# Kernel optimization log

Measured on AMD Instinct MI355X. Metric: run time of the kernel, lower is better.

The kernel has to match this reference:

```python
import jax, jax.numpy as jnp
import numpy as np

# ---- module constants (from init_kwargs / zounds.SR22050) ----
SEQ = 64
N_SAMPLES = 16384
N_EVENTS = 16
N_HARM = 32
NOISE_WS = 512
NOISE_STEP = 256
NYQ = 11025.0  # SR22050 nyquist
MIN_F0 = 20.0 / NYQ
MAX_F0 = 800.0 / NYQ
F0_DIFF = MAX_F0 - MIN_F0
HARM_FACTOR = jnp.arange(2, 2 + N_HARM, dtype=jnp.float32)  # [2..33]


def lin_interp(x, size):
    """torch F.interpolate(mode='linear', align_corners=False) along last dim."""
    L = x.shape[-1]
    pos = (jnp.arange(size, dtype=x.dtype) + 0.5) * (L / size) - 0.5
    pos = jnp.clip(pos, 0.0, L - 1)
    i0 = jnp.floor(pos).astype(jnp.int32)
    i1 = jnp.minimum(i0 + 1, L - 1)
    w = (pos - i0).astype(x.dtype)
    return x[..., i0] * (1.0 - w) + x[..., i1] * w


def band_filtered_noise(noise_frames, mean, std):
    """Per-frame Gaussian band-pass of white noise in the STFT domain, overlap-add.
    noise_frames: (b,e,F,ws); mean/std: (b,e,F) in normalized freq [0,1]."""
    ws = noise_frames.shape[-1]
    n = jnp.arange(ws, dtype=noise_frames.dtype)
    win = 0.5 - 0.5 * jnp.cos(2.0 * jnp.pi * n / ws)  # Hann
    spec = jnp.fft.rfft(noise_frames * win, axis=-1)  # (b,e,F,ws//2+1)
    freqs = jnp.linspace(0.0, 1.0, ws // 2 + 1)
    filt = jnp.exp(-0.5 * ((freqs[None, None, None, :] - mean[..., None]) / std[..., None]) ** 2)
    frames = jnp.fft.irfft(spec * filt, n=ws, axis=-1)  # (b,e,F,ws)
    # overlap-add with hop NOISE_STEP (ws == 2*step -> two half-chunks per frame)
    b, e, Fn, _ = frames.shape
    chunks = frames.reshape(b, e, Fn, 2, NOISE_STEP)
    a = chunks[..., 0, :].reshape(b, e, Fn * NOISE_STEP)
    c = chunks[..., 1, :].reshape(b, e, Fn * NOISE_STEP)
    out = jnp.zeros((b, e, (Fn + 1) * NOISE_STEP), dtype=frames.dtype)
    out = out.at[..., : Fn * NOISE_STEP].add(a)
    out = out.at[..., NOISE_STEP:].add(c)
    return out[..., :N_SAMPLES]


def setup_inputs() -> dict:
    key = jax.random.key(0)
    ks = jax.random.split(key, 8)
    B = 8
    return {
        "f0": jax.random.uniform(ks[0], (B, N_EVENTS, SEQ), jnp.float32),
        "overall_env": jax.random.uniform(ks[1], (B, N_EVENTS, SEQ), jnp.float32),
        "osc_env": jax.random.uniform(ks[2], (B, N_EVENTS, SEQ), jnp.float32),
        "noise_env": jax.random.uniform(ks[3], (B, N_EVENTS, SEQ), jnp.float32),
        "harm_env": jax.random.uniform(ks[4], (B, N_EVENTS, N_HARM, SEQ), jnp.float32),
        "noise_std": jax.random.uniform(ks[5], (B, N_EVENTS, SEQ), jnp.float32),
        "f0_baselines": jax.random.uniform(ks[6], (B, N_EVENTS, 1), jnp.float32),
        "noise_frames": jax.random.normal(ks[7], (B, N_EVENTS, SEQ, NOISE_WS), jnp.float32),
    }


def reference(f0, overall_env, osc_env, noise_env, harm_env, noise_std, f0_baselines, noise_frames):
    # f0_baselines branch (ERB-scaled deviation around baseline)
    f0 = jnp.clip(f0, -0.5, 0.5)
    scaled_erb = (0.108 * (f0_baselines * NYQ) + 24.7) / NYQ
    f0 = f0_baselines + f0 * scaled_erb

    orig_f0 = f0 = jnp.clip(f0, 0.0, 1.0)
    overall_env = jnp.clip(overall_env, 0.0, 1.0)
    osc_env = jnp.clip(osc_env, 0.0, 1.0)
    harm_env = jnp.clip(harm_env, 0.0, 1.0)
    noise_std = jnp.clip(noise_std, 1e-12, 1.0)

    f0n = MIN_F0 + f0 * F0_DIFF                                   # (b,e,S)
    harm_f = f0n[:, :, None, :] * HARM_FACTOR[None, None, :, None]  # (b,e,H,S)
    harm_env = osc_env[:, :, None, :] * harm_env                  # (b,e,H,S)

    fund = lin_interp(f0n, N_SAMPLES)           # (b,e,N)
    harm_f_i = lin_interp(harm_f, N_SAMPLES)    # (b,e,H,N)
    osc_env_i = lin_interp(osc_env, N_SAMPLES)  # (b,e,N)
    harm_env_i = lin_interp(harm_env, N_SAMPLES)

    fundamental = jnp.sin(jnp.cumsum(fund * jnp.pi, axis=-1)) * osc_env_i
    harmonics = (jnp.sin(jnp.cumsum(harm_f_i * jnp.pi, axis=-1)) * harm_env_i).sum(axis=-2)
    osc = fundamental + harmonics

    noise_mean = MIN_F0 + orig_f0 * F0_DIFF
    nstd = noise_std * F0_DIFF
    noise = band_filtered_noise(noise_frames, noise_mean, nstd)

    osc_mix = lin_interp(overall_env, N_SAMPLES)
    noise_mix = lin_interp(1.0 - overall_env, N_SAMPLES)
    return osc * osc_mix + noise * noise_mix
```

## Files before the change

kernel.cpp:

```cpp
#include <hip/hip_runtime.h>
#include <math.h>

#define SEQ 64
#define NSAMP 16384
#define NHARM 32
#define NWS 512
#define NSTEP 256
#define BE 128
#define NFRAMES 8192

typedef _Float16 half8 __attribute__((ext_vector_type(8)));
typedef float f32x4 __attribute__((ext_vector_type(4)));

__device__ __forceinline__ float sin_rev(float x) {
  float r; asm("v_sin_f32 %0, %1" : "=v"(r) : "v"(x)); return r;
}
__device__ __forceinline__ float cos_rev(float x) {
  float r; asm("v_cos_f32 %0, %1" : "=v"(r) : "v"(x)); return r;
}
__device__ __forceinline__ float clip01(float v) { return fminf(fmaxf(v, 0.0f), 1.0f); }

__device__ __forceinline__ float f0_to_norm(float f0v, float bl) {
  const float NYQ = 11025.0f;
  const float MIN_F0 = 20.0f / 11025.0f;
  const float F0_DIFF = 780.0f / 11025.0f;
  float v = fminf(fmaxf(f0v, -0.5f), 0.5f);
  float erb = (0.108f * (bl * NYQ) + 24.7f) / NYQ;
  float fv = clip01(bl + v * erb);
  return MIN_F0 + fv * F0_DIFF;
}

__global__ __launch_bounds__(256) void prep_k(_Float16* __restrict__ W1) {
  const int m = blockIdx.x, k = m & 127;
  const int tid = threadIdx.x;
  const bool isSin = m >= 128;
  for (int n = tid; n < 512; n += 256) {
    int a = (k * n) & 511;
    float ph = (float)a * (1.0f / 512.0f);
    W1[m * 512 + n] = (_Float16)(isSin ? sin_rev(ph) : cos_rev(ph));
  }
}

__global__ __launch_bounds__(256) void gemmf_k(const float* __restrict__ Af,
                                               const _Float16* __restrict__ B,
                                               _Float16* __restrict__ Cout,
                                               _Float16* __restrict__ W2,
                                               const float* __restrict__ f0,
                                               const float* __restrict__ nstd,
                                               const float* __restrict__ f0b) {
  const int tid = threadIdx.x;

  if (blockIdx.x < 256) {
    const int k = tid & 127;
    const bool isSin = tid >= 128;
#pragma unroll
    for (int rr = 0; rr < 2; ++rr) {
      const int n = blockIdx.x * 2 + rr;
      int a = (k * n) & 511;
      float ph = (float)a * (1.0f / 512.0f);
      W2[n * 256 + tid] = (_Float16)(isSin ? sin_rev(ph) : cos_rev(ph));
    }
    return;
  }

  const int p = blockIdx.x - 256;
  const int x = p & 7, j = p >> 3;
  const int mstripe = ((j >> 2) << 3) + x;
  const int bn0 = (j & 3) * 64;
  const int m0 = mstripe * 32;

  const int Kt = 512;
  const int wave = tid >> 6, lane = tid & 63;
  const int r = lane & 15, q = lane >> 4;
  const int wr = (wave & 1) * 16;
  const int wc = (wave >> 1) * 32;
  __shared__ __align__(16) _Float16 Ash[2][32 * 64];
  __shared__ __align__(16) _Float16 Bsh[2][64 * 64];
  __shared__ __align__(16) float whann[512];

  const int nT = Kt >> 6;
  const int srowA = tid >> 3;
  const int srowB0 = tid >> 3, srowB1 = (256 + tid) >> 3;
  const int skg = tid & 7;

  half8 ra, rb[2];
  f32x4 acc[2] = {};

  whann[tid] = 0.5f - 0.5f * cos_rev((float)tid * (1.0f / 512.0f));
  whann[tid + 256] = 0.5f - 0.5f * cos_rev((float)(tid + 256) * (1.0f / 512.0f));
  __syncthreads();

  auto load_a = [&](int kk) {
    const float* s0 = Af + (size_t)(m0 + srowA) * Kt + kk + skg * 8;
    float4 a0 = ((const float4*)s0)[0], a1 = ((const float4*)s0)[1];
    float4 w0 = *(const float4*)(&whann[kk + skg * 8]);
    float4 w1 = *(const float4*)(&whann[kk + skg * 8 + 4]);
    ra[0] = (_Float16)(a0.x * w0.x); ra[1] = (_Float16)(a0.y * w0.y);
    ra[2] = (_Float16)(a0.z * w0.z); ra[3] = (_Float16)(a0.w * w0.w);
    ra[4] = (_Float16)(a1.x * w1.x); ra[5] = (_Float16)(a1.y * w1.y);
    ra[6] = (_Float16)(a1.z * w1.z); ra[7] = (_Float16)(a1.w * w1.w);
    rb[0] = *(const half8*)(B + (size_t)(bn0 + srowB0) * Kt + kk + skg * 8);
    rb[1] = *(const half8*)(B + (size_t)(bn0 + srowB1) * Kt + kk + skg * 8);
  };
  auto store_lds = [&](int b) {
    *(half8*)(&Ash[b][srowA * 64 + ((skg ^ (srowA & 7)) << 3)]) = ra;
    *(half8*)(&Bsh[b][srowB0 * 64 + ((skg ^ (srowB0 & 7)) << 3)]) = rb[0];
    *(half8*)(&Bsh[b][srowB1 * 64 + ((skg ^ (srowB1 & 7)) << 3)]) = rb[1];
  };

  load_a(0);
  store_lds(0);

  for (int t = 0;;) {
    if (t + 1 < nT) load_a((t + 1) << 6);
    __syncthreads();
    const int b = t & 1;
#pragma unroll
    for (int ks = 0; ks < 2; ++ks) {
      const int kg = ks * 4 + q;
      const int ar = wr + r;
      half8 af = *(const half8*)(&Ash[b][ar * 64 + ((kg ^ (ar & 7)) << 3)]);
#pragma unroll
      for (int ni = 0; ni < 2; ++ni) {
        const int br = wc + ni * 16 + r;
        half8 bf = *(const half8*)(&Bsh[b][br * 64 + ((kg ^ (br & 7)) << 3)]);
        acc[ni] = __builtin_amdgcn_mfma_f32_16x16x32_f16(af, bf, acc[ni], 0, 0, 0);
      }
    }
    if (t + 1 >= nT) break;
    __syncthreads();
    store_lds((t + 1) & 1);
    ++t;
  }

  const float F0_DIFF = 780.0f / 11025.0f;
#pragma unroll
  for (int reg = 0; reg < 4; ++reg) {
    const int row = m0 + wr + q * 4 + reg;
    const float mu = f0_to_norm(f0[row], f0b[row >> 6]);
    const float sd = fminf(fmaxf(nstd[row], 1e-12f), 1.0f) * F0_DIFF;
    const float inv_sd = 1.0f / sd;
    const float a = inv_sd * (1.0f / 256.0f);
    const float bmu = mu * inv_sd;
#pragma unroll
    for (int ni = 0; ni < 2; ++ni) {
      const int col = bn0 + wc + ni * 16 + r;
      const int k = col & 127;
      float z = fmaf((float)k, a, -bmu);
      float cf = (k == 0) ? (1.0f / 512.0f) : (2.0f / 512.0f);
      float s = cf * exp2f(z * z * -0.72134752044f);
      Cout[(size_t)row * 256 + col] = (_Float16)(acc[ni][reg] * s);
    }
  }
}

__global__ __launch_bounds__(256) void invfin_k(const _Float16* __restrict__ AB,
                                                const _Float16* __restrict__ W2,
                                                const float* __restrict__ f0,
                                                const float* __restrict__ f0b,
                                                const float* __restrict__ oenv_g,
                                                const float* __restrict__ oscenv_g,
                                                const float* __restrict__ henv_g,
                                                float* __restrict__ out) {
  const int p = blockIdx.x;
  const int x = p & 7, j = p >> 3;
  const int be = ((j >> 3) << 3) + x;
  const int sub = j & 7;
  const int chalf = sub >> 2;
  const int n0 = (sub & 3) * 64;
  const int m0c = be * 64 + chalf * 32;
  const int tid = threadIdx.x;
  const int wave = tid >> 6, lane = tid & 63;
  const int r = lane & 15, q = lane >> 4;
  const int wr = (wave & 1) * 16;
  const int wc = (wave >> 1) * 32;

  __shared__ __align__(16) _Float16 A2sh[33 * 64];
  __shared__ __align__(16) _Float16 B1sh[64 * 64];
  __shared__ __align__(16) _Float16 B2sh[64 * 64];
  __shared__ __align__(16) float4 qe4[8 * SEQ];
  __shared__ float oenv[SEQ], oscE[SEQ];
  __shared__ float Fs[SEQ], Ds[SEQ], Gs[SEQ];

  if (tid < SEQ) {
    oenv[tid] = clip01(oenv_g[be * SEQ + tid]);
    oscE[tid] = clip01(oscenv_g[be * SEQ + tid]);
    Fs[tid] = f0_to_norm(f0[be * SEQ + tid], f0b[be]);
  }
  __syncthreads();

  if (tid < SEQ) {
    const int s = tid;
    float fcur = Fs[s];
    float fnxt = (s < 63) ? Fs[s + 1] : Fs[63];
    Ds[s] = fnxt - fcur;
    double term = 128.0 * ((double)fcur + (double)fnxt);
    double sc = term;
#pragma unroll
    for (int off = 1; off < 64; off <<= 1) {
      double u = __shfl_up(sc, off, 64);
      if (s >= off) sc += u;
    }
    double C = 128.0 * (double)Fs[0] + (sc - term);
    Gs[s] = (float)(C - 2.0 * floor(C * 0.5));
  }

  for (int idx = tid; idx < 8 * SEQ; idx += 256) {
    int hq = idx >> 6, s = idx & 63;
    const float* hb = henv_g + (size_t)be * (NHARM * SEQ) + (4 * hq) * SEQ + s;
    float e = oscE[s];
    qe4[idx] = make_float4(e * clip01(hb[0]), e * clip01(hb[64]),
                           e * clip01(hb[128]), e * clip01(hb[192]));
  }

  auto stage_AB = [&](int kk) {
#pragma unroll
    for (int it = 0; it < 2; ++it) {
      int g = it * 256 + tid;
      if (g < 264) {
        int row = g >> 3, kg = g & 7;
        half8 v = {0, 0, 0, 0, 0, 0, 0, 0};
        if (row > 0 || chalf == 1)
          v = *(const half8*)(AB + (size_t)(m0c - 1 + row) * 256 + kk + kg * 8);
        *(half8*)(&A2sh[row * 64 + ((kg ^ (row & 7)) << 3)]) = v;
      }
    }
#pragma unroll
    for (int it = 0; it < 4; ++it) {
      int g = it * 256 + tid;
      int row = (g >> 3) & 63, kg = g & 7;
      bool second = g >= 512;
      int wrow = n0 + row + (second ? 256 : 0);
      half8 v = *(const half8*)(W2 + (size_t)wrow * 256 + kk + kg * 8);
      _Float16* dst = second ? B2sh : B1sh;
      *(half8*)(&dst[row * 64 + ((kg ^ (row & 7)) << 3)]) = v;
    }
  };

  f32x4 acc[2] = {};
  stage_AB(0);
  __syncthreads();

  for (int t = 0;;) {
#pragma unroll
    for (int ks = 0; ks < 2; ++ks) {
      const int kg = ks * 4 + q;
      const int ra1 = 1 + wr + r;
      const int ra2 = wr + r;
      half8 af1 = *(const half8*)(&A2sh[ra1 * 64 + ((kg ^ (ra1 & 7)) << 3)]);
      half8 af2 = *(const half8*)(&A2sh[ra2 * 64 + ((kg ^ (ra2 & 7)) << 3)]);
#pragma unroll
      for (int ni = 0; ni < 2; ++ni) {
        const int rb = wc + ni * 16 + r;
        const int sw = (kg ^ (rb & 7)) << 3;
        half8 bf1 = *(const half8*)(&B1sh[rb * 64 + sw]);
        half8 bf2 = *(const half8*)(&B2sh[rb * 64 + sw]);
        acc[ni] = __builtin_amdgcn_mfma_f32_16x16x32_f16(af1, bf1, acc[ni], 0, 0, 0);
        acc[ni] = __builtin_amdgcn_mfma_f32_16x16x32_f16(af2, bf2, acc[ni], 0, 0, 0);
      }
    }
    if (t == 3) break;
    __syncthreads();
    stage_AB((t + 1) << 6);
    __syncthreads();
    ++t;
  }

#pragma unroll
  for (int reg = 0; reg < 4; ++reg) {
    const int c = chalf * 32 + wr + q * 4 + reg;
#pragma unroll
    for (int ni = 0; ni < 2; ++ni) {
      const int n = n0 + wc + ni * 16 + r;
      const int t = c * 256 + n;
      float pos = ((float)t + 0.5f) * (1.0f / 256.0f) - 0.5f;
      pos = fminf(fmaxf(pos, 0.0f), 63.0f);
      int i0 = (int)pos;
      int i1 = min(i0 + 1, 63);
      float w = pos - (float)i0;

      float pph;
      if (t < 128) {
        pph = (float)(t + 1) * Fs[0];
      } else {
        int s = (t - 128) >> 8;
        float u1 = (float)((t - 128) - (s << 8) + 1);
        pph = Gs[s] + fmaf(Ds[s] * (1.0f / 512.0f), u1 * u1, u1 * Fs[s]);
      }
      pph = pph - 2.0f * floorf(pph * 0.5f);
      float xv = pph * 0.5f;
      float sb = sin_rev(xv);
      float cb = cos_rev(xv);
      float C = 2.0f * cb;

      float fund = sb * (oscE[i0] * (1.0f - w) + oscE[i1] * w);
      float d0 = 0.0f, d1 = 0.0f;
      float sp = sb;
      float scur = C * sb;
#pragma unroll
      for (int hq = 0; hq < 8; ++hq) {
        float4 qa = qe4[hq * 64 + i0];
        float4 qb = qe4[hq * 64 + i1];
        d0 = fmaf(scur, qa.x, d0); d1 = fmaf(scur, qb.x, d1);
        sp = fmaf(C, scur, -sp);
        d0 = fmaf(sp, qa.y, d0);   d1 = fmaf(sp, qb.y, d1);
        scur = fmaf(C, sp, -scur);
        d0 = fmaf(scur, qa.z, d0); d1 = fmaf(scur, qb.z, d1);
        sp = fmaf(C, scur, -sp);
        d0 = fmaf(sp, qa.w, d0);   d1 = fmaf(sp, qb.w, d1);
        scur = fmaf(C, sp, -scur);
      }
      float osc = fund + d0 * (1.0f - w) + d1 * w;
      float mix = oenv[i0] * (1.0f - w) + oenv[i1] * w;
      out[(size_t)be * NSAMP + t] = fmaf(osc, mix, acc[ni][reg] * (1.0f - mix));
    }
  }
}

extern "C" void kernel_launch(void* const* d_in, const int* in_sizes, int n_in,
                              void* d_out, int out_size, void* d_ws, size_t ws_size,
                              hipStream_t stream) {
  const float* f0           = (const float*)d_in[0];
  const float* overall_env  = (const float*)d_in[1];
  const float* osc_env      = (const float*)d_in[2];
  const float* harm_env     = (const float*)d_in[4];
  const float* noise_std    = (const float*)d_in[5];
  const float* f0_base      = (const float*)d_in[6];
  const float* noise_frames = (const float*)d_in[7];
  float* out = (float*)d_out;

  _Float16* W1 = (_Float16*)d_ws;
  _Float16* W2 = W1 + 256 * 512;
  _Float16* AB = W2 + 512 * 256;

  prep_k<<<256, 256, 0, stream>>>(W1);
  gemmf_k<<<1280, 256, 0, stream>>>(noise_frames, W1, AB, W2, f0, noise_std, f0_base);
  invfin_k<<<1024, 256, 0, stream>>>(
      AB, W2, f0, f0_base, overall_env, osc_env, harm_env, out);
}
```

Baseline: 34.54 us.

## Generate DFT twiddles inline in forward GEMM and prefetch inverse GEMM tiles

Removes the separate prep kernel that wrote the forward DFT matrix to global memory. The forward GEMM now computes its cos/sin B-tile values on the fly with hardware sin/cos instructions while the A tile is being loaded. Separately, the inverse GEMM staging is split into a global-load phase issued before the MFMA loop and an LDS-write phase afterward, so loads overlap compute. This saves a kernel launch and global traffic but adds 16 transcendental ops per thread per tile in the forward GEMM.

```diff
diff --git a/kernel.cpp b/kernel.cpp
--- a/kernel.cpp
+++ b/kernel.cpp
@@ -30,19 +30,7 @@
   return MIN_F0 + fv * F0_DIFF;
 }
 
-__global__ __launch_bounds__(256) void prep_k(_Float16* __restrict__ W1) {
-  const int m = blockIdx.x, k = m & 127;
-  const int tid = threadIdx.x;
-  const bool isSin = m >= 128;
-  for (int n = tid; n < 512; n += 256) {
-    int a = (k * n) & 511;
-    float ph = (float)a * (1.0f / 512.0f);
-    W1[m * 512 + n] = (_Float16)(isSin ? sin_rev(ph) : cos_rev(ph));
-  }
-}
-
 __global__ __launch_bounds__(256) void gemmf_k(const float* __restrict__ Af,
-                                               const _Float16* __restrict__ B,
                                                _Float16* __restrict__ Cout,
                                                _Float16* __restrict__ W2,
                                                const float* __restrict__ f0,
@@ -89,6 +77,11 @@
   whann[tid] = 0.5f - 0.5f * cos_rev((float)tid * (1.0f / 512.0f));
   whann[tid + 256] = 0.5f - 0.5f * cos_rev((float)(tid + 256) * (1.0f / 512.0f));
   __syncthreads();
+
+  const int kB0 = (bn0 + srowB0) & 127;
+  const int kB1 = (bn0 + srowB1) & 127;
+  const bool sB0 = (bn0 + srowB0) >= 128;
+  const bool sB1 = (bn0 + srowB1) >= 128;
 
   auto load_a = [&](int kk) {
     const float* s0 = Af + (size_t)(m0 + srowA) * Kt + kk + skg * 8;
@@ -99,8 +92,17 @@
     ra[2] = (_Float16)(a0.z * w0.z); ra[3] = (_Float16)(a0.w * w0.w);
     ra[4] = (_Float16)(a1.x * w1.x); ra[5] = (_Float16)(a1.y * w1.y);
     ra[6] = (_Float16)(a1.z * w1.z); ra[7] = (_Float16)(a1.w * w1.w);
-    rb[0] = *(const half8*)(B + (size_t)(bn0 + srowB0) * Kt + kk + skg * 8);
-    rb[1] = *(const half8*)(B + (size_t)(bn0 + srowB1) * Kt + kk + skg * 8);
+  };
+  auto gen_b = [&](int kk) {
+    const int nbase = kk + skg * 8;
+#pragma unroll
+    for (int jj = 0; jj < 8; ++jj) {
+      const int n = nbase + jj;
+      float ph0 = (float)((kB0 * n) & 511) * (1.0f / 512.0f);
+      float ph1 = (float)((kB1 * n) & 511) * (1.0f / 512.0f);
+      rb[0][jj] = (_Float16)(sB0 ? sin_rev(ph0) : cos_rev(ph0));
+      rb[1][jj] = (_Float16)(sB1 ? sin_rev(ph1) : cos_rev(ph1));
+    }
   };
   auto store_lds = [&](int b) {
     *(half8*)(&Ash[b][srowA * 64 + ((skg ^ (srowA & 7)) << 3)]) = ra;
@@ -109,10 +111,11 @@
   };
 
   load_a(0);
+  gen_b(0);
   store_lds(0);
 
   for (int t = 0;;) {
-    if (t + 1 < nT) load_a((t + 1) << 6);
+    if (t + 1 < nT) { load_a((t + 1) << 6); gen_b((t + 1) << 6); }
     __syncthreads();
     const int b = t & 1;
 #pragma unroll
@@ -213,35 +216,48 @@
                            e * clip01(hb[128]), e * clip01(hb[192]));
   }
 
-  auto stage_AB = [&](int kk) {
-#pragma unroll
-    for (int it = 0; it < 2; ++it) {
-      int g = it * 256 + tid;
-      if (g < 264) {
-        int row = g >> 3, kg = g & 7;
-        half8 v = {0, 0, 0, 0, 0, 0, 0, 0};
-        if (row > 0 || chalf == 1)
-          v = *(const half8*)(AB + (size_t)(m0c - 1 + row) * 256 + kk + kg * 8);
-        *(half8*)(&A2sh[row * 64 + ((kg ^ (row & 7)) << 3)]) = v;
-      }
-    }
+  half8 raA0, raA1, rbB[4];
+  const int rowA0 = tid >> 3, kgA0 = tid & 7;
+  const int rowA1 = (256 + tid) >> 3, kgA1 = tid & 7;
+
+  auto stage_load = [&](int kk) {
+    {
+      half8 v = {0, 0, 0, 0, 0, 0, 0, 0};
+      if (rowA0 > 0 || chalf == 1)
+        v = *(const half8*)(AB + (size_t)(m0c - 1 + rowA0) * 256 + kk + kgA0 * 8);
+      raA0 = v;
+    }
+    if (tid < 8)
+      raA1 = *(const half8*)(AB + (size_t)(m0c - 1 + rowA1) * 256 + kk + kgA1 * 8);
 #pragma unroll
     for (int it = 0; it < 4; ++it) {
       int g = it * 256 + tid;
-      int row = (g >> 3) & 63, kg = g & 7;
+      int row = (g >> 3) & 63;
       bool second = g >= 512;
       int wrow = n0 + row + (second ? 256 : 0);
-      half8 v = *(const half8*)(W2 + (size_t)wrow * 256 + kk + kg * 8);
-      _Float16* dst = second ? B2sh : B1sh;
-      *(half8*)(&dst[row * 64 + ((kg ^ (row & 7)) << 3)]) = v;
+      rbB[it] = *(const half8*)(W2 + (size_t)wrow * 256 + kk + (g & 7) * 8);
+    }
+  };
+  auto stage_write = [&]() {
+    *(half8*)(&A2sh[rowA0 * 64 + ((kgA0 ^ (rowA0 & 7)) << 3)]) = raA0;
+    if (tid < 8)
+      *(half8*)(&A2sh[rowA1 * 64 + ((kgA1 ^ (rowA1 & 7)) << 3)]) = raA1;
+#pragma unroll
+    for (int it = 0; it < 4; ++it) {
+      int g = it * 256 + tid;
+      int row = (g >> 3) & 63;
+      _Float16* dst = (g >= 512) ? B2sh : B1sh;
+      *(half8*)(&dst[row * 64 + (((g & 7) ^ (row & 7)) << 3)]) = rbB[it];
     }
   };
 
   f32x4 acc[2] = {};
-  stage_AB(0);
+  stage_load(0);
+  stage_write();
   __syncthreads();
 
   for (int t = 0;;) {
+    if (t < 3) stage_load((t + 1) << 6);
 #pragma unroll
     for (int ks = 0; ks < 2; ++ks) {
       const int kg = ks * 4 + q;
@@ -261,7 +277,7 @@
     }
     if (t == 3) break;
     __syncthreads();
-    stage_AB((t + 1) << 6);
+    stage_write();
     __syncthreads();
     ++t;
   }
@@ -329,12 +345,10 @@
   const float* noise_frames = (const float*)d_in[7];
   float* out = (float*)d_out;
 
-  _Float16* W1 = (_Float16*)d_ws;
-  _Float16* W2 = W1 + 256 * 512;
+  _Float16* W2 = (_Float16*)d_ws;
   _Float16* AB = W2 + 512 * 256;
 
-  prep_k<<<256, 256, 0, stream>>>(W1);
-  gemmf_k<<<1280, 256, 0, stream>>>(noise_frames, W1, AB, W2, f0, noise_std, f0_base);
+  gemmf_k<<<1280, 256, 0, stream>>>(noise_frames, AB, W2, f0, noise_std, f0_base);
   invfin_k<<<1024, 256, 0, stream>>>(
       AB, W2, f0, f0_base, overall_env, osc_env, harm_env, out);
 }
```

Result: faster. 33.53 us (-2.9%).
